# Performance work log

Measured on AMD Instinct MI355X. Metric: run time of the kernel, lower is better.

The kernel has to match this reference:

```python
import jax, jax.numpy as jnp
import numpy as np


def setup_inputs() -> dict:
    key = jax.random.key(0)
    k1, k2, k3 = jax.random.split(key, 3)
    B, N, D = 8, 4096, 64
    q = jax.random.normal(k1, (B, N, D), dtype=jnp.float32)
    k = jax.random.normal(k2, (B, N, D), dtype=jnp.float32)
    v = jax.random.normal(k3, (B, N, D), dtype=jnp.float32)
    attn_mask = jnp.ones((B, N), dtype=jnp.int32)  # 1 = attend, 0 = padding
    return {"q": q, "k": k, "v": v, "attn_mask": attn_mask}


def reference(q, k, v, attn_mask):
    # q: [B, n_q, d], k/v: [B, n_k, d], attn_mask: [B, n_k]
    d = q.shape[-1]
    n_q, n_k = q.shape[1], k.shape[1]
    scale = jnp.sqrt(jnp.asarray(d, dtype=q.dtype))
    # [B, n_q, n_k] attention logits
    logits = jnp.einsum("bqd,bkd->bqk", q, k) / scale
    # causal (mask_future=True): tril keep-mask over (n_q, n_k)
    causal = jnp.tril(jnp.ones((n_q, n_k), dtype=bool))
    neg_inf = jnp.asarray(-jnp.inf, dtype=logits.dtype)
    logits = jnp.where(causal[None, :, :], logits, neg_inf)
    # padding mask broadcast over query dim: [B, 1, n_k]
    logits = jnp.where(attn_mask[:, None, :] == 0, neg_inf, logits)
    w = jax.nn.softmax(logits, axis=-1)
    return jnp.einsum("bqk,bkd->bqd", w, v)
```

## Files before the change

### kernel.cpp

```cpp
#include <hip/hip_runtime.h>


#define BATCH 8
#define SEQ   4096
#define DIM   64
#define QT    64
#define NKT   (SEQ / 64)

typedef __attribute__((ext_vector_type(8))) short bf16x8;
typedef __attribute__((ext_vector_type(4))) float f32x4;
typedef __attribute__((ext_vector_type(4))) unsigned u32x4;

__device__ inline short f2bf(float f) {
    unsigned u = __builtin_bit_cast(unsigned, f);
    u += 0x7FFFu + ((u >> 16) & 1u);
    return (short)(u >> 16);
}

__device__ inline unsigned pk2bf(float a, float b) {
    unsigned ua = __builtin_bit_cast(unsigned, a) + 0x8000u;
    unsigned ub = __builtin_bit_cast(unsigned, b) + 0x8000u;
    return __builtin_amdgcn_perm(ub, ua, 0x07060302u);
}

__device__ inline float fast_exp2(float x) {
#if __has_builtin(__builtin_amdgcn_exp2f)
    return __builtin_amdgcn_exp2f(x);
#else
    return exp2f(x);
#endif
}

__device__ inline void gl_lds16(const void* g, void* l) {
    __builtin_amdgcn_global_load_lds(
        (const __attribute__((address_space(1))) void*)g,
        (__attribute__((address_space(3))) void*)l, 16, 0, 0);
}

__global__ __launch_bounds__(256)
void prep_kv(const float* __restrict__ kg, const float* __restrict__ vg,
             const int* __restrict__ mg, short* __restrict__ kw,
             short* __restrict__ vw, float* __restrict__ mf) {
    const int tile = blockIdx.x;
    const float* kp = kg + (size_t)tile * 64 * DIM;
    const float* vp = vg + (size_t)tile * 64 * DIM;
    short* ko = kw + (size_t)tile * 4096;
    short* vo = vw + (size_t)tile * 4096;
    const int t = threadIdx.x;
    if (mf && t < 64) {
        const int* mp = mg + (size_t)tile * 64;
        mf[(size_t)tile * 64 + t] = mp[t] ? 0.0f : -1e30f;
    }
#pragma unroll
    for (int i = 0; i < 4; ++i) {
        const int flat = i * 256 + t;
        const int key = flat >> 4, d0 = (flat & 15) * 4;
        const float4 kv = *(const float4*)(kp + (size_t)key * DIM + d0);
        uint2 kpk;
        kpk.x = pk2bf(kv.x, kv.y); kpk.y = pk2bf(kv.z, kv.w);
        *(uint2*)(ko + (((d0 >> 3) << 6) + key) * 8 + (d0 & 7)) = kpk;
        const float4 vv = *(const float4*)(vp + (size_t)key * DIM + d0);
        const int vcell = ((key >> 5) << 2) | ((key >> 2) & 3);
        const int vj    = (((key >> 4) & 1) << 2) | (key & 3);
        vo[((vcell << 6) + d0 + 0) * 8 + vj] = f2bf(vv.x);
        vo[((vcell << 6) + d0 + 1) * 8 + vj] = f2bf(vv.y);
        vo[((vcell << 6) + d0 + 2) * 8 + vj] = f2bf(vv.z);
        vo[((vcell << 6) + d0 + 3) * 8 + vj] = f2bf(vv.w);
    }
}

__global__ __launch_bounds__(512, 8)
void attn_split4(const float* __restrict__ qg, float* __restrict__ og,
                 const short* __restrict__ kw, const short* __restrict__ vw,
                 const float* __restrict__ mf, float* __restrict__ opart,
                 float* __restrict__ lpart) {
    __shared__ __align__(16) char smem[32768];
    short* KbS = (short*)smem;
    short* VbS = (short*)(smem + 16384);
    float* OX = (float*)smem;
    float* LB = (float*)(smem + 16384);

    const int t    = threadIdx.x;
    const int w    = t >> 6;
    const int L    = t & 63;
    const int c15  = L & 15;
    const int quad = L >> 4;
    const int qsub = w & 3;
    const int kh   = w >> 2;

    const int id  = blockIdx.x;
    const int b   = id & 7;
    const int r_  = id >> 3;
    const int j   = r_ & 31;
    const int ch  = r_ >> 5;
    const int nL  = 64 - j;
    const int qLt = 63 - j;

    const float* qp  = qg + (size_t)b * SEQ * DIM;
    const float* mb  = mf + (size_t)b * SEQ;
    const short* kwb = kw + (size_t)b * NKT * 4096;
    const short* vwb = vw + (size_t)b * NKT * 4096;
    float* osl = opart + (size_t)(b * 32 + j) * 12288;
    float* lsl = lpart + (size_t)(b * 32 + j) * 384;
    const float qscale = 0.125f * 1.44269504088896340736f;

    auto stage = [&](int bs, int kt) {
        const short* ks = kwb + (size_t)kt * 4096;
        const short* vs = vwb + (size_t)kt * 4096;
        const int off = w << 9;
        gl_lds16(ks + off + (L << 3), KbS + bs * 4096 + off);
        gl_lds16(vs + off + (L << 3), VbS + bs * 4096 + off);
    };

    int sqt[2], sk0[2], sk1[2], smode[2], sos[2], sls[2], nseg;
    sos[0] = sos[1] = 0; sls[0] = sls[1] = 0;
    if (ch == 0) {
        nseg = 1;
        sqt[0] = qLt; sk0[0] = 0;  sk1[0] = 16; smode[0] = 0; sls[0] = 0;
    } else if (ch == 1) {
        nseg = 1;
        sqt[0] = qLt; sk0[0] = 16; sk1[0] = 32; smode[0] = 1; sos[0] = 0; sls[0] = 1;
    } else if (ch == 2) {
        if (nL >= 48) {
            nseg = 1;
            sqt[0] = qLt; sk0[0] = 32; sk1[0] = 48; smode[0] = 1; sos[0] = 1; sls[0] = 2;
        } else {
            nseg = 2;
            sqt[0] = qLt; sk0[0] = 32; sk1[0] = nL;      smode[0] = 1; sos[0] = 1; sls[0] = 2;
            sqt[1] = j;   sk0[1] = 0;  sk1[1] = 48 - nL; smode[1] = 0; sls[1] = 4;
        }
    } else {
        if (nL > 48) {
            nseg = 2;
            sqt[0] = qLt; sk0[0] = 48; sk1[0] = nL;    smode[0] = 1; sos[0] = 2; sls[0] = 3;
            sqt[1] = j;   sk0[1] = 0;  sk1[1] = j + 1; smode[1] = 2;
        } else if (nL == 48) {
            nseg = 1;
            sqt[0] = j; sk0[0] = 0; sk1[0] = j + 1; smode[0] = 2;
        } else {
            nseg = 1;
            sqt[0] = j; sk0[0] = 48 - nL; sk1[0] = j + 1; smode[0] = 1; sos[0] = 2; sls[0] = 5;
        }
    }

    for (int seg = 0; seg < nseg; ++seg) {
        const int qt   = sqt[seg];
        const int kt0  = sk0[seg];
        const int kt1  = sk1[seg];
        const int mode = smode[seg];

        const int qbase = qt * QT;
        const int qrow  = qbase + qsub * 16 + c15;

        bf16x8 Qf[2];
#pragma unroll
        for (int c = 0; c < 2; ++c) {
            const float* src = qp + (size_t)qrow * DIM + c * 32 + quad * 8;
            float4 x = *(const float4*)(src);
            float4 y = *(const float4*)(src + 4);
            bf16x8 f;
            f[0] = f2bf(x.x * qscale); f[1] = f2bf(x.y * qscale);
            f[2] = f2bf(x.z * qscale); f[3] = f2bf(x.w * qscale);
            f[4] = f2bf(y.x * qscale); f[5] = f2bf(y.y * qscale);
            f[6] = f2bf(y.z * qscale); f[7] = f2bf(y.w * qscale);
            Qf[c] = f;
        }

        float lsum = 0.0f;
        f32x4 Oacc[4];
#pragma unroll
        for (int nb = 0; nb < 4; ++nb) Oacc[nb] = (f32x4){0.f, 0.f, 0.f, 0.f};

        stage(0, kt0);

        for (int kt = kt0; kt < kt1; ++kt) {
            const int cur = (kt - kt0) & 1;
            __syncthreads();
            if (kt + 1 < kt1) stage(cur ^ 1, kt + 1);

            const short* Kt = KbS + cur * 4096;
            const short* Vt = VbS + cur * 4096;

            f32x4 sacc[2];
            sacc[0] = (f32x4){0.f, 0.f, 0.f, 0.f};
            sacc[1] = (f32x4){0.f, 0.f, 0.f, 0.f};
#pragma unroll
            for (int c = 0; c < 2; ++c) {
#pragma unroll
                for (int i = 0; i < 2; ++i) {
                    bf16x8 kf = *(const bf16x8*)&Kt[(((quad + 4 * c) << 6) + (2 * kh + i) * 16 + c15) * 8];
                    sacc[i] = __builtin_amdgcn_mfma_f32_16x16x32_bf16(kf, Qf[c], sacc[i], 0, 0, 0);
                }
            }

            const bool diag = (kt == qt);
            unsigned pu[4];
#pragma unroll
            for (int i = 0; i < 2; ++i) {
                const int kb = 2 * kh + i;
                const float4 ma = *(const float4*)&mb[kt * 64 + kb * 16 + quad * 4];
                const float mar[4] = {ma.x, ma.y, ma.z, ma.w};
                float p[4];
#pragma unroll
                for (int r = 0; r < 4; ++r) {
                    float s = sacc[i][r] + mar[r];
                    if (diag) {
                        const int keyg = kt * 64 + kb * 16 + quad * 4 + r;
                        if (keyg > qrow) s = -1e30f;
                    }
                    p[r] = fast_exp2(fminf(s, 80.0f));
                    lsum += p[r];
                }
                pu[2 * i]     = pk2bf(p[0], p[1]);
                pu[2 * i + 1] = pk2bf(p[2], p[3]);
            }

            const bf16x8 pf = __builtin_bit_cast(bf16x8,
                (u32x4){pu[0], pu[1], pu[2], pu[3]});
#pragma unroll
            for (int nb = 0; nb < 4; ++nb) {
                bf16x8 vf = *(const bf16x8*)&Vt[(((kh * 4 + quad) << 6) + nb * 16 + c15) * 8];
                Oacc[nb] = __builtin_amdgcn_mfma_f32_16x16x32_bf16(pf, vf, Oacc[nb], 0, 0, 0);
            }
        }

        lsum += __shfl_xor(lsum, 16);
        lsum += __shfl_xor(lsum, 32);

        __syncthreads();
        if (w >= 4) {
            const int g = w & 3;
#pragma unroll
            for (int r = 0; r < 4; ++r) {
                const int q = quad * 4 + r;
#pragma unroll
                for (int nb = 0; nb < 4; ++nb)
                    OX[(g * 16 + q) * 64 + nb * 16 + c15] = Oacc[nb][r];
            }
            if (quad == 0) LB[g * 16 + c15] = lsum;
        }
        __syncthreads();
        if (w < 4) {
            const float ltot = lsum + LB[w * 16 + c15];
            const float inv  = 1.0f / ltot;
            float* dst = (mode == 1) ? osl + (size_t)sos[seg] * 4096
                                     : og + ((size_t)b * SEQ + qbase) * DIM;
            if (mode != 2 && L < 16)
                lsl[sls[seg] * 64 + w * 16 + L] = ltot;
#pragma unroll
            for (int r = 0; r < 4; ++r) {
                const float ir = (mode == 2)
                    ? __shfl(inv, (L & 48) + ((L & 48) >> 2) + r) : 1.0f;
                const int rl = w * 16 + quad * 4 + r;
#pragma unroll
                for (int nb = 0; nb < 4; ++nb)
                    dst[(size_t)rl * DIM + nb * 16 + c15] =
                        (Oacc[nb][r] + OX[rl * 64 + nb * 16 + c15]) * ir;
            }
        }
        __syncthreads();
    }
}

__global__ __launch_bounds__(256)
void merge4(float* __restrict__ og, const float* __restrict__ opart,
            const float* __restrict__ lpart) {
    const int id = blockIdx.x;
    const int b = id & 7, j = id >> 3;
    const int nL = 64 - j, qLt = 63 - j;
    const float* os = opart + (size_t)(b * 32 + j) * 12288;
    const float* ls = lpart + (size_t)(b * 32 + j) * 384;
    const int t = threadIdx.x;
    const bool has3 = (nL > 48);

    float* opL = og + ((size_t)b * SEQ + (size_t)qLt * 64) * DIM;
#pragma unroll
    for (int i = 0; i < 4; ++i) {
        const int flat = i * 256 + t;
        const int row = flat >> 4;
        const int c4  = (flat & 15) * 4;
        float l = ls[row] + ls[64 + row] + ls[128 + row];
        if (has3) l += ls[192 + row];
        const float inv = 1.0f / l;
        const float4 a  = *(const float4*)(opL + (size_t)row * DIM + c4);
        const float4 p0 = *(const float4*)(os + (size_t)row * 64 + c4);
        const float4 p1 = *(const float4*)(os + 4096 + (size_t)row * 64 + c4);
        float sx = a.x + p0.x + p1.x;
        float sy = a.y + p0.y + p1.y;
        float sz = a.z + p0.z + p1.z;
        float sw = a.w + p0.w + p1.w;
        if (has3) {
            const float4 p2 = *(const float4*)(os + 8192 + (size_t)row * 64 + c4);
            sx += p2.x; sy += p2.y; sz += p2.z; sw += p2.w;
        }
        float4 r;
        r.x = sx * inv; r.y = sy * inv; r.z = sz * inv; r.w = sw * inv;
        *(float4*)(opL + (size_t)row * DIM + c4) = r;
    }

    if (nL < 48) {
        float* opS = og + ((size_t)b * SEQ + (size_t)j * 64) * DIM;
#pragma unroll
        for (int i = 0; i < 4; ++i) {
            const int flat = i * 256 + t;
            const int row = flat >> 4;
            const int c4  = (flat & 15) * 4;
            const float inv = 1.0f / (ls[256 + row] + ls[320 + row]);
            const float4 a  = *(const float4*)(opS + (size_t)row * DIM + c4);
            const float4 p2 = *(const float4*)(os + 8192 + (size_t)row * 64 + c4);
            float4 r;
            r.x = (a.x + p2.x) * inv;
            r.y = (a.y + p2.y) * inv;
            r.z = (a.z + p2.z) * inv;
            r.w = (a.w + p2.w) * inv;
            *(float4*)(opS + (size_t)row * DIM + c4) = r;
        }
    }
}

template <bool WS>
__global__ __launch_bounds__(512, 4)
void attn_fwd(const float* __restrict__ qg, const float* __restrict__ kg,
              const float* __restrict__ vg, const int* __restrict__ mg,
              float* __restrict__ og, const short* __restrict__ kw,
              const short* __restrict__ vw) {
    __shared__ __align__(16) char smem[59392];
    short* KbS = (short*)smem;
    short* VbS = (short*)(smem + 16384);
    float* Ml  = (float*)(smem + 43008);
    float* OX = (float*)smem;
    float* LB = (float*)(smem + 16384);

    const int t    = threadIdx.x;
    const int w    = t >> 6;
    const int L    = t & 63;
    const int c15  = L & 15;
    const int quad = L >> 4;
    const int qsub = w & 3;
    const int kh   = w >> 2;

    const int id = blockIdx.x;
    const int b  = id & 7;
    const int j  = id >> 3;
    const int qb = (j < 32) ? (63 - j) : (j - 32);
    const int qbase  = qb * QT;
    const int ntiles = qb + 1;

    const float* qp = qg + (size_t)b * SEQ * DIM;
    const float* kp = kg + (size_t)b * SEQ * DIM;
    const float* vp = vg + (size_t)b * SEQ * DIM;
    const int*   mp = mg + (size_t)b * SEQ;
    const short* kwb = WS ? kw + (size_t)b * NKT * 4096 : nullptr;
    const short* vwb = WS ? vw + (size_t)b * NKT * 4096 : nullptr;

    const int qrow = qbase + qsub * 16 + c15;
    const float qscale = 0.125f * 1.44269504088896340736f;

    bf16x8 Qf[2];
#pragma unroll
    for (int c = 0; c < 2; ++c) {
        const float* src = qp + (size_t)qrow * DIM + c * 32 + quad * 8;
        float4 x = *(const float4*)(src);
        float4 y = *(const float4*)(src + 4);
        bf16x8 f;
        f[0] = f2bf(x.x * qscale); f[1] = f2bf(x.y * qscale);
        f[2] = f2bf(x.z * qscale); f[3] = f2bf(x.w * qscale);
        f[4] = f2bf(y.x * qscale); f[5] = f2bf(y.y * qscale);
        f[6] = f2bf(y.z * qscale); f[7] = f2bf(y.w * qscale);
        Qf[c] = f;
    }

    auto stage = [&](int bs, int kt) {
        const short* ks = kwb + (size_t)kt * 4096;
        const short* vs = vwb + (size_t)kt * 4096;
        const int off = w << 9;
        gl_lds16(ks + off + (L << 3), KbS + bs * 4096 + off);
        gl_lds16(vs + off + (L << 3), VbS + bs * 4096 + off);
    };

    for (int i = t; i < ntiles * 64; i += 512)
        Ml[i] = mp[i] ? 0.0f : -1e30f;

    float lsum = 0.0f;
    f32x4 Oacc[4];
#pragma unroll
    for (int nb = 0; nb < 4; ++nb) Oacc[nb] = (f32x4){0.f, 0.f, 0.f, 0.f};

    if constexpr (WS) stage(0, 0);

    for (int kt = 0; kt < ntiles; ++kt) {
        const int cur = WS ? (kt & 1) : 0;

        if constexpr (!WS) {
            __syncthreads();
#pragma unroll
            for (int it = 0; it < 2; ++it) {
                const int flat = it * 512 + t;
                const int key = flat >> 4, d0 = (flat & 15) * 4;
                const float4 kv = *(const float4*)(kp + (size_t)(kt * 64 + key) * DIM + d0);
                uint2 kk;
                kk.x = pk2bf(kv.x, kv.y); kk.y = pk2bf(kv.z, kv.w);
                *(uint2*)&KbS[(((d0 >> 3) << 6) + key) * 8 + (d0 & 7)] = kk;
                const float4 vv = *(const float4*)(vp + (size_t)(kt * 64 + key) * DIM + d0);
                const int vcell = ((key >> 5) << 2) | ((key >> 2) & 3);
                const int vj    = (((key >> 4) & 1) << 2) | (key & 3);
                VbS[((vcell << 6) + d0 + 0) * 8 + vj] = f2bf(vv.x);
                VbS[((vcell << 6) + d0 + 1) * 8 + vj] = f2bf(vv.y);
                VbS[((vcell << 6) + d0 + 2) * 8 + vj] = f2bf(vv.z);
                VbS[((vcell << 6) + d0 + 3) * 8 + vj] = f2bf(vv.w);
            }
            __syncthreads();
        } else {
            __syncthreads();
            if (kt + 1 < ntiles) stage(cur ^ 1, kt + 1);
        }

        const short* Kt = KbS + cur * 4096;
        const short* Vt = VbS + cur * 4096;

        f32x4 sacc[2];
        sacc[0] = (f32x4){0.f, 0.f, 0.f, 0.f};
        sacc[1] = (f32x4){0.f, 0.f, 0.f, 0.f};
#pragma unroll
        for (int c = 0; c < 2; ++c) {
#pragma unroll
            for (int i = 0; i < 2; ++i) {
                bf16x8 kf = *(const bf16x8*)&Kt[(((quad + 4 * c) << 6) + (2 * kh + i) * 16 + c15) * 8];
                sacc[i] = __builtin_amdgcn_mfma_f32_16x16x32_bf16(kf, Qf[c], sacc[i], 0, 0, 0);
            }
        }

        const bool diag = (kt == ntiles - 1);
        unsigned pu[4];
#pragma unroll
        for (int i = 0; i < 2; ++i) {
            const int kb = 2 * kh + i;
            const float4 ma = *(const float4*)&Ml[kt * 64 + kb * 16 + quad * 4];
            const float mar[4] = {ma.x, ma.y, ma.z, ma.w};
            float p[4];
#pragma unroll
            for (int r = 0; r < 4; ++r) {
                float s = sacc[i][r] + mar[r];
                if (diag) {
                    const int keyg = kt * 64 + kb * 16 + quad * 4 + r;
                    if (keyg > qrow) s = -1e30f;
                }
                p[r] = fast_exp2(fminf(s, 80.0f));
                lsum += p[r];
            }
            pu[2 * i]     = pk2bf(p[0], p[1]);
            pu[2 * i + 1] = pk2bf(p[2], p[3]);
        }

        const bf16x8 pf = __builtin_bit_cast(bf16x8,
            (u32x4){pu[0], pu[1], pu[2], pu[3]});
#pragma unroll
        for (int nb = 0; nb < 4; ++nb) {
            bf16x8 vf = *(const bf16x8*)&Vt[(((kh * 4 + quad) << 6) + nb * 16 + c15) * 8];
            Oacc[nb] = __builtin_amdgcn_mfma_f32_16x16x32_bf16(pf, vf, Oacc[nb], 0, 0, 0);
        }
    }

    lsum += __shfl_xor(lsum, 16);
    lsum += __shfl_xor(lsum, 32);

    __syncthreads();
    if (w >= 4) {
        const int g = w & 3;
#pragma unroll
        for (int r = 0; r < 4; ++r) {
            const int q = quad * 4 + r;
#pragma unroll
            for (int nb = 0; nb < 4; ++nb)
                OX[(g * 16 + q) * 64 + nb * 16 + c15] = Oacc[nb][r];
        }
        if (quad == 0) LB[g * 16 + c15] = lsum;
    }
    __syncthreads();
    if (w < 4) {
        const float inv = 1.0f / (lsum + LB[w * 16 + c15]);
        float* op = og + (size_t)b * SEQ * DIM;
#pragma unroll
        for (int r = 0; r < 4; ++r) {
            const float ir = __shfl(inv, (L & 48) + ((L & 48) >> 2) + r);
            const int row = qbase + w * 16 + quad * 4 + r;
#pragma unroll
            for (int nb = 0; nb < 4; ++nb)
                op[(size_t)row * DIM + nb * 16 + c15] =
                    (Oacc[nb][r] + OX[(w * 16 + quad * 4 + r) * 64 + nb * 16 + c15]) * ir;
        }
    }
}

extern "C" void kernel_launch(void* const* d_in, const int* in_sizes, int n_in,
                              void* d_out, int out_size, void* d_ws, size_t ws_size,
                              hipStream_t stream) {
    (void)in_sizes; (void)n_in; (void)out_size;
    const float* q = (const float*)d_in[0];
    const float* k = (const float*)d_in[1];
    const float* v = (const float*)d_in[2];
    const int*   m = (const int*)d_in[3];
    float* o = (float*)d_out;

    const size_t kvB    = (size_t)BATCH * NKT * 4096 * sizeof(short);
    const size_t maddB  = (size_t)BATCH * SEQ * sizeof(float);
    const size_t opartB = (size_t)BATCH * 32 * 12288 * sizeof(float);
    const size_t lpartB = (size_t)BATCH * 32 * 384 * sizeof(float);
    const size_t need4  = 2 * kvB + maddB + opartB + lpartB;

    if (ws_size >= need4) {
        short* kw = (short*)d_ws;
        short* vw = kw + (size_t)BATCH * NKT * 4096;
        float* mf = (float*)((char*)d_ws + 2 * kvB);
        float* opart = (float*)((char*)d_ws + 2 * kvB + maddB);
        float* lpart = opart + (size_t)BATCH * 32 * 12288;
        prep_kv<<<dim3(BATCH * NKT), 256, 0, stream>>>(k, v, m, kw, vw, mf);
        attn_split4<<<dim3(1024), 512, 0, stream>>>(q, o, kw, vw, mf, opart, lpart);
        merge4<<<dim3(256), 256, 0, stream>>>(o, opart, lpart);
    } else if (ws_size >= 2 * kvB) {
        short* kw = (short*)d_ws;
        short* vw = kw + (size_t)BATCH * NKT * 4096;
        prep_kv<<<dim3(BATCH * NKT), 256, 0, stream>>>(k, v, m, kw, vw, nullptr);
        attn_fwd<true><<<dim3(512), 512, 0, stream>>>(q, k, v, m, o, kw, vw);
    } else {
        attn_fwd<false><<<dim3(512), 512, 0, stream>>>(q, k, v, m, o, nullptr, nullptr);
    }
}
```

Baseline: 131.3 us.

## Process two query sub-tiles per wave with 256-thread blocks and MFMA row sums

Halves the attention block to 4 waves, each handling 32 query rows (two 16-row sub-tiles) against a key half, so every K/V fragment read from LDS feeds two MFMAs. The row-sum of probabilities moves from scalar adds plus shuffles to an MFMA against a ones vector. The mask is preloaded into the score accumulator, and the clamp before exp2 is dropped. It also adds setprio around MFMA sections, replaces the barrier with an explicit waitcnt, and uses nontemporal loads in the prep kernel. In exchange it raises register pressure per wave and gives fewer waves per block to hide latency.

```diff
diff --git a/kernel.cpp b/kernel.cpp
--- a/kernel.cpp
+++ b/kernel.cpp
@@ -35,6 +35,10 @@
     __builtin_amdgcn_global_load_lds(
         (const __attribute__((address_space(1))) void*)g,
         (__attribute__((address_space(3))) void*)l, 16, 0, 0);
+}
+
+__device__ inline f32x4 ntl4(const float* p) {
+    return __builtin_nontemporal_load((const f32x4*)p);
 }
 
 __global__ __launch_bounds__(256)
@@ -55,28 +59,27 @@
     for (int i = 0; i < 4; ++i) {
         const int flat = i * 256 + t;
         const int key = flat >> 4, d0 = (flat & 15) * 4;
-        const float4 kv = *(const float4*)(kp + (size_t)key * DIM + d0);
+        const f32x4 kv = ntl4(kp + (size_t)key * DIM + d0);
         uint2 kpk;
-        kpk.x = pk2bf(kv.x, kv.y); kpk.y = pk2bf(kv.z, kv.w);
+        kpk.x = pk2bf(kv[0], kv[1]); kpk.y = pk2bf(kv[2], kv[3]);
         *(uint2*)(ko + (((d0 >> 3) << 6) + key) * 8 + (d0 & 7)) = kpk;
-        const float4 vv = *(const float4*)(vp + (size_t)key * DIM + d0);
+        const f32x4 vv = ntl4(vp + (size_t)key * DIM + d0);
         const int vcell = ((key >> 5) << 2) | ((key >> 2) & 3);
         const int vj    = (((key >> 4) & 1) << 2) | (key & 3);
-        vo[((vcell << 6) + d0 + 0) * 8 + vj] = f2bf(vv.x);
-        vo[((vcell << 6) + d0 + 1) * 8 + vj] = f2bf(vv.y);
-        vo[((vcell << 6) + d0 + 2) * 8 + vj] = f2bf(vv.z);
-        vo[((vcell << 6) + d0 + 3) * 8 + vj] = f2bf(vv.w);
-    }
-}
-
-__global__ __launch_bounds__(512, 8)
+        vo[((vcell << 6) + d0 + 0) * 8 + vj] = f2bf(vv[0]);
+        vo[((vcell << 6) + d0 + 1) * 8 + vj] = f2bf(vv[1]);
+        vo[((vcell << 6) + d0 + 2) * 8 + vj] = f2bf(vv[2]);
+        vo[((vcell << 6) + d0 + 3) * 8 + vj] = f2bf(vv[3]);
+    }
+}
+
+__global__ __launch_bounds__(256, 4)
 void attn_split4(const float* __restrict__ qg, float* __restrict__ og,
                  const short* __restrict__ kw, const short* __restrict__ vw,
                  const float* __restrict__ mf, float* __restrict__ opart,
                  float* __restrict__ lpart) {
     __shared__ __align__(16) char smem[32768];
     short* KbS = (short*)smem;
-    short* VbS = (short*)(smem + 16384);
     float* OX = (float*)smem;
     float* LB = (float*)(smem + 16384);
 
@@ -85,8 +88,8 @@
     const int L    = t & 63;
     const int c15  = L & 15;
     const int quad = L >> 4;
-    const int qsub = w & 3;
-    const int kh   = w >> 2;
+    const int qgrp = w >> 1;
+    const int kh   = w & 1;
 
     const int id  = blockIdx.x;
     const int b   = id & 7;
@@ -107,10 +110,17 @@
     auto stage = [&](int bs, int kt) {
         const short* ks = kwb + (size_t)kt * 4096;
         const short* vs = vwb + (size_t)kt * 4096;
-        const int off = w << 9;
-        gl_lds16(ks + off + (L << 3), KbS + bs * 4096 + off);
-        gl_lds16(vs + off + (L << 3), VbS + bs * 4096 + off);
+        const int off = w << 10;
+        short* base = KbS + bs * 8192;
+        gl_lds16(ks + off +       (L << 3), base + off);
+        gl_lds16(ks + off + 512 + (L << 3), base + off + 512);
+        gl_lds16(vs + off +       (L << 3), base + 4096 + off);
+        gl_lds16(vs + off + 512 + (L << 3), base + 4096 + off + 512);
     };
+
+    bf16x8 vones;
+#pragma unroll
+    for (int z = 0; z < 8; ++z) vones[z] = (short)0x3F80;
 
     int sqt[2], sk0[2], sk1[2], smode[2], sos[2], sls[2], nseg;
     sos[0] = sos[1] = 0; sls[0] = sls[1] = 0;
@@ -150,112 +160,145 @@
         const int mode = smode[seg];
 
         const int qbase = qt * QT;
-        const int qrow  = qbase + qsub * 16 + c15;
-
-        bf16x8 Qf[2];
-#pragma unroll
-        for (int c = 0; c < 2; ++c) {
-            const float* src = qp + (size_t)qrow * DIM + c * 32 + quad * 8;
-            float4 x = *(const float4*)(src);
-            float4 y = *(const float4*)(src + 4);
-            bf16x8 f;
-            f[0] = f2bf(x.x * qscale); f[1] = f2bf(x.y * qscale);
-            f[2] = f2bf(x.z * qscale); f[3] = f2bf(x.w * qscale);
-            f[4] = f2bf(y.x * qscale); f[5] = f2bf(y.y * qscale);
-            f[6] = f2bf(y.z * qscale); f[7] = f2bf(y.w * qscale);
-            Qf[c] = f;
-        }
-
-        float lsum = 0.0f;
-        f32x4 Oacc[4];
-#pragma unroll
-        for (int nb = 0; nb < 4; ++nb) Oacc[nb] = (f32x4){0.f, 0.f, 0.f, 0.f};
+        int qrow[2];
+        qrow[0] = qbase + qgrp * 32 + c15;
+        qrow[1] = qrow[0] + 16;
+
+        bf16x8 Qf[2][2];
+#pragma unroll
+        for (int s = 0; s < 2; ++s) {
+#pragma unroll
+            for (int c = 0; c < 2; ++c) {
+                const float* src = qp + (size_t)qrow[s] * DIM + c * 32 + quad * 8;
+                float4 x = *(const float4*)(src);
+                float4 y = *(const float4*)(src + 4);
+                bf16x8 f;
+                f[0] = f2bf(x.x * qscale); f[1] = f2bf(x.y * qscale);
+                f[2] = f2bf(x.z * qscale); f[3] = f2bf(x.w * qscale);
+                f[4] = f2bf(y.x * qscale); f[5] = f2bf(y.y * qscale);
+                f[6] = f2bf(y.z * qscale); f[7] = f2bf(y.w * qscale);
+                Qf[s][c] = f;
+            }
+        }
+        asm volatile("" ::: "memory");
+
+        f32x4 lacc[2];
+        lacc[0] = (f32x4){0.f, 0.f, 0.f, 0.f};
+        lacc[1] = (f32x4){0.f, 0.f, 0.f, 0.f};
+        f32x4 Oacc[2][4];
+#pragma unroll
+        for (int s = 0; s < 2; ++s)
+#pragma unroll
+            for (int nb = 0; nb < 4; ++nb)
+                Oacc[s][nb] = (f32x4){0.f, 0.f, 0.f, 0.f};
 
         stage(0, kt0);
+        int cur = 0;
+        const float* mrow = mb + (size_t)kt0 * 64 + (2 * kh) * 16 + quad * 4;
 
         for (int kt = kt0; kt < kt1; ++kt) {
-            const int cur = (kt - kt0) & 1;
-            __syncthreads();
+            asm volatile("s_waitcnt vmcnt(0)" ::: "memory");
+            __builtin_amdgcn_s_barrier();
+            asm volatile("" ::: "memory");
+
+            const float4 ma0 = *(const float4*)(mrow);
+            const float4 ma1 = *(const float4*)(mrow + 16);
+            mrow += 64;
+            asm volatile("" ::: "memory");
             if (kt + 1 < kt1) stage(cur ^ 1, kt + 1);
 
-            const short* Kt = KbS + cur * 4096;
-            const short* Vt = VbS + cur * 4096;
-
-            f32x4 sacc[2];
-            sacc[0] = (f32x4){0.f, 0.f, 0.f, 0.f};
-            sacc[1] = (f32x4){0.f, 0.f, 0.f, 0.f};
+            const short* Kt = KbS + cur * 8192;
+            const short* Vt = Kt + 4096;
+            cur ^= 1;
+
+            f32x4 sacc[2][2];
+#pragma unroll
+            for (int s = 0; s < 2; ++s) {
+                sacc[s][0] = (f32x4){ma0.x, ma0.y, ma0.z, ma0.w};
+                sacc[s][1] = (f32x4){ma1.x, ma1.y, ma1.z, ma1.w};
+            }
+            __builtin_amdgcn_s_setprio(1);
 #pragma unroll
             for (int c = 0; c < 2; ++c) {
 #pragma unroll
                 for (int i = 0; i < 2; ++i) {
                     bf16x8 kf = *(const bf16x8*)&Kt[(((quad + 4 * c) << 6) + (2 * kh + i) * 16 + c15) * 8];
-                    sacc[i] = __builtin_amdgcn_mfma_f32_16x16x32_bf16(kf, Qf[c], sacc[i], 0, 0, 0);
+#pragma unroll
+                    for (int s = 0; s < 2; ++s)
+                        sacc[s][i] = __builtin_amdgcn_mfma_f32_16x16x32_bf16(kf, Qf[s][c], sacc[s][i], 0, 0, 0);
                 }
             }
+            __builtin_amdgcn_s_setprio(0);
 
             const bool diag = (kt == qt);
-            unsigned pu[4];
-#pragma unroll
-            for (int i = 0; i < 2; ++i) {
-                const int kb = 2 * kh + i;
-                const float4 ma = *(const float4*)&mb[kt * 64 + kb * 16 + quad * 4];
-                const float mar[4] = {ma.x, ma.y, ma.z, ma.w};
-                float p[4];
-#pragma unroll
-                for (int r = 0; r < 4; ++r) {
-                    float s = sacc[i][r] + mar[r];
-                    if (diag) {
-                        const int keyg = kt * 64 + kb * 16 + quad * 4 + r;
-                        if (keyg > qrow) s = -1e30f;
+            bf16x8 pf[2];
+#pragma unroll
+            for (int s = 0; s < 2; ++s) {
+                unsigned pu[4];
+#pragma unroll
+                for (int i = 0; i < 2; ++i) {
+                    float p[4];
+#pragma unroll
+                    for (int r = 0; r < 4; ++r) {
+                        float sv = sacc[s][i][r];
+                        if (diag) {
+                            const int keyg = kt * 64 + (2 * kh + i) * 16 + quad * 4 + r;
+                            if (keyg > qrow[s]) sv = -1e30f;
+                        }
+                        p[r] = fast_exp2(sv);
                     }
-                    p[r] = fast_exp2(fminf(s, 80.0f));
-                    lsum += p[r];
+                    pu[2 * i]     = pk2bf(p[0], p[1]);
+                    pu[2 * i + 1] = pk2bf(p[2], p[3]);
                 }
-                pu[2 * i]     = pk2bf(p[0], p[1]);
-                pu[2 * i + 1] = pk2bf(p[2], p[3]);
-            }
-
-            const bf16x8 pf = __builtin_bit_cast(bf16x8,
-                (u32x4){pu[0], pu[1], pu[2], pu[3]});
+                pf[s] = __builtin_bit_cast(bf16x8,
+                    (u32x4){pu[0], pu[1], pu[2], pu[3]});
+            }
+
+            __builtin_amdgcn_s_setprio(1);
 #pragma unroll
             for (int nb = 0; nb < 4; ++nb) {
                 bf16x8 vf = *(const bf16x8*)&Vt[(((kh * 4 + quad) << 6) + nb * 16 + c15) * 8];
-                Oacc[nb] = __builtin_amdgcn_mfma_f32_16x16x32_bf16(pf, vf, Oacc[nb], 0, 0, 0);
-            }
-        }
-
-        lsum += __shfl_xor(lsum, 16);
-        lsum += __shfl_xor(lsum, 32);
+#pragma unroll
+                for (int s = 0; s < 2; ++s)
+                    Oacc[s][nb] = __builtin_amdgcn_mfma_f32_16x16x32_bf16(pf[s], vf, Oacc[s][nb], 0, 0, 0);
+            }
+            lacc[0] = __builtin_amdgcn_mfma_f32_16x16x32_bf16(pf[0], vones, lacc[0], 0, 0, 0);
+            lacc[1] = __builtin_amdgcn_mfma_f32_16x16x32_bf16(pf[1], vones, lacc[1], 0, 0, 0);
+            __builtin_amdgcn_s_setprio(0);
+        }
 
         __syncthreads();
-        if (w >= 4) {
-            const int g = w & 3;
-#pragma unroll
-            for (int r = 0; r < 4; ++r) {
-                const int q = quad * 4 + r;
-#pragma unroll
-                for (int nb = 0; nb < 4; ++nb)
-                    OX[(g * 16 + q) * 64 + nb * 16 + c15] = Oacc[nb][r];
-            }
-            if (quad == 0) LB[g * 16 + c15] = lsum;
+        if (kh == 1) {
+#pragma unroll
+            for (int s = 0; s < 2; ++s) {
+#pragma unroll
+                for (int r = 0; r < 4; ++r) {
+                    const int rl = qgrp * 32 + s * 16 + quad * 4 + r;
+#pragma unroll
+                    for (int nb = 0; nb < 4; ++nb)
+                        OX[rl * 64 + nb * 16 + c15] = Oacc[s][nb][r];
+                    if (c15 == 0) LB[rl] = lacc[s][r];
+                }
+            }
         }
         __syncthreads();
-        if (w < 4) {
-            const float ltot = lsum + LB[w * 16 + c15];
-            const float inv  = 1.0f / ltot;
+        if (kh == 0) {
             float* dst = (mode == 1) ? osl + (size_t)sos[seg] * 4096
                                      : og + ((size_t)b * SEQ + qbase) * DIM;
-            if (mode != 2 && L < 16)
-                lsl[sls[seg] * 64 + w * 16 + L] = ltot;
-#pragma unroll
-            for (int r = 0; r < 4; ++r) {
-                const float ir = (mode == 2)
-                    ? __shfl(inv, (L & 48) + ((L & 48) >> 2) + r) : 1.0f;
-                const int rl = w * 16 + quad * 4 + r;
-#pragma unroll
-                for (int nb = 0; nb < 4; ++nb)
-                    dst[(size_t)rl * DIM + nb * 16 + c15] =
-                        (Oacc[nb][r] + OX[rl * 64 + nb * 16 + c15]) * ir;
+#pragma unroll
+            for (int s = 0; s < 2; ++s) {
+#pragma unroll
+                for (int r = 0; r < 4; ++r) {
+                    const int rl = qgrp * 32 + s * 16 + quad * 4 + r;
+                    const float lt = lacc[s][r] + LB[rl];
+                    const float ir = (mode == 2) ? 1.0f / lt : 1.0f;
+                    if (mode != 2 && c15 == 0)
+                        lsl[sls[seg] * 64 + rl] = lt;
+#pragma unroll
+                    for (int nb = 0; nb < 4; ++nb)
+                        dst[(size_t)rl * DIM + nb * 16 + c15] =
+                            (Oacc[s][nb][r] + OX[rl * 64 + nb * 16 + c15]) * ir;
+                }
             }
         }
         __syncthreads();
@@ -515,7 +558,7 @@
         float* opart = (float*)((char*)d_ws + 2 * kvB + maddB);
         float* lpart = opart + (size_t)BATCH * 32 * 12288;
         prep_kv<<<dim3(BATCH * NKT), 256, 0, stream>>>(k, v, m, kw, vw, mf);
-        attn_split4<<<dim3(1024), 512, 0, stream>>>(q, o, kw, vw, mf, opart, lpart);
+        attn_split4<<<dim3(1024), 256, 0, stream>>>(q, o, kw, vw, mf, opart, lpart);
         merge4<<<dim3(256), 256, 0, stream>>>(o, opart, lpart);
     } else if (ws_size >= 2 * kvB) {
         short* kw = (short*)d_ws;
```

Result: faster. 122.3 us (-6.8%).
